# Kernel tuning notes

Measured on AMD Instinct MI355X. Metric: run time of the kernel, lower is better.

## Reference

```python
import jax, jax.numpy as jnp
import numpy as np

DIM = 1024
NUM_HEADS = 16
HEAD_DIM = DIM // NUM_HEADS
BATCH = 64
SEQ = 256


def rope_tables(seq_len, head_dim, dtype=jnp.float32):
    inv_freq = 1.0 / (10000.0 ** (jnp.arange(0, head_dim, 2, dtype=jnp.float32) / head_dim))
    pos = jnp.arange(seq_len, dtype=jnp.float32)
    freqs = jnp.outer(pos, inv_freq)            # (S, head_dim/2)
    emb = jnp.concatenate([freqs, freqs], -1)   # (S, head_dim)
    return jnp.cos(emb).astype(dtype), jnp.sin(emb).astype(dtype)


def rotate_half(x):
    x1, x2 = jnp.split(x, 2, axis=-1)
    return jnp.concatenate([-x2, x1], axis=-1)


def setup_inputs() -> dict:
    key = jax.random.key(0)
    ks = jax.random.split(key, 5)
    x = jax.random.normal(ks[0], (BATCH, SEQ, DIM), dtype=jnp.float32)
    mask = jnp.ones((BATCH, SEQ), dtype=jnp.int32)
    s = 1.0 / np.sqrt(DIM)
    Wq = jax.random.normal(ks[1], (DIM, DIM), dtype=jnp.float32) * s
    Wk = jax.random.normal(ks[2], (DIM, DIM), dtype=jnp.float32) * s
    Wv = jax.random.normal(ks[3], (DIM, DIM), dtype=jnp.float32) * s
    Wo = jax.random.normal(ks[4], (DIM, DIM), dtype=jnp.float32) * s
    return {"x": x, "mask": mask, "Wq": Wq, "Wk": Wk, "Wv": Wv, "Wo": Wo}


def reference(x, mask, Wq, Wk, Wv, Wo):
    B, S, D = x.shape
    H, Hd = NUM_HEADS, HEAD_DIM
    scale = Hd ** -0.5
    # torch nn.Linear: y = x @ W^T  (weights stored as (out,in))
    q = (x @ Wq.T).reshape(B, S, H, Hd).transpose(0, 2, 1, 3)  # (B,H,S,Hd)
    k = (x @ Wk.T).reshape(B, S, H, Hd).transpose(0, 2, 1, 3)
    v = (x @ Wv.T).reshape(B, S, H, Hd).transpose(0, 2, 1, 3)
    cos, sin = rope_tables(S, Hd, x.dtype)       # (S,Hd)
    cos = cos[None, None]                         # (1,1,S,Hd)
    sin = sin[None, None]
    q = q * cos + rotate_half(q) * sin
    k = k * cos + rotate_half(k) * sin
    scores = jnp.einsum('bhqd,bhkd->bhqk', q, k) * scale  # (B,H,S,S)
    m = (mask[:, None, None, :] != 0)             # (B,1,1,S)
    scores = jnp.where(m, scores, -jnp.inf)
    attn = jax.nn.softmax(scores, axis=-1)
    out = jnp.einsum('bhqk,bhkd->bhqd', attn, v)  # (B,H,S,Hd)
    out = out.transpose(0, 2, 1, 3).reshape(B, S, D)
    return out @ Wo.T
```

## Files before the change

### kernel.cpp

```cpp
#include <hip/hip_runtime.h>

typedef __attribute__((ext_vector_type(8))) short short8;
typedef __attribute__((ext_vector_type(4))) float f32x4;

#define DEV __device__ __forceinline__

DEV unsigned short f2bf(float f) {
    unsigned int u = __float_as_uint(f);
    u += 0x7FFFu + ((u >> 16) & 1u);
    return (unsigned short)(u >> 16);
}
DEV float bf2f(unsigned short h) { return __uint_as_float(((unsigned int)h) << 16); }

DEV void gload16(const void* g, void* l) {
    __builtin_amdgcn_global_load_lds(
        (const __attribute__((address_space(1))) void*)(unsigned long long)g,
        (__attribute__((address_space(3))) void*)(unsigned int)(unsigned long long)l,
        16, 0, 0);
}

DEV void cast8(const float* in, unsigned short* out, size_t idx8) {
    const f32x4* p = (const f32x4*)in + idx8 * 2;
    f32x4 a = p[0], b = p[1];
    short8 v;
    v[0] = (short)f2bf(a[0]); v[1] = (short)f2bf(a[1]); v[2] = (short)f2bf(a[2]); v[3] = (short)f2bf(a[3]);
    v[4] = (short)f2bf(b[0]); v[5] = (short)f2bf(b[1]); v[6] = (short)f2bf(b[2]); v[7] = (short)f2bf(b[3]);
    *(short8*)(out + idx8 * 8) = v;
}

__global__ void init_kernel(const float* __restrict__ x,
                            const float* __restrict__ w0, const float* __restrict__ w1,
                            const float* __restrict__ w2, const float* __restrict__ w3,
                            unsigned short* __restrict__ xb,
                            unsigned short* __restrict__ o0, unsigned short* __restrict__ o1,
                            unsigned short* __restrict__ o2, unsigned short* __restrict__ o3,
                            float* __restrict__ cosT, float* __restrict__ sinT) {
    int blk = blockIdx.x;
    int tid = threadIdx.x;
    if (blk < 8192) {
        cast8(x, xb, (size_t)blk * 256 + tid);
    } else if (blk < 8192 + 2048) {
        int gid = (blk - 8192) * 256 + tid;
        int sel = gid >> 17, idx = gid & 131071;
        const float* in = (sel == 0) ? w0 : (sel == 1) ? w1 : (sel == 2) ? w2 : w3;
        unsigned short* out = (sel == 0) ? o0 : (sel == 1) ? o1 : (sel == 2) ? o2 : o3;
        cast8(in, out, (size_t)idx);
    } else {
        int gid = (blk - 8192 - 2048) * 256 + tid;
        if (gid < 256 * 32) {
            int s = gid >> 5, i = gid & 31;
            float inv = powf(10000.0f, -(float)i * (1.0f / 32.0f));
            float f = (float)s * inv;
            cosT[gid] = cosf(f);
            sinT[gid] = sinf(f);
        }
    }
}

#define NT0 16

#define Ald(B, K) (SLDS + ((B) * 2 + (K)) * 8192)
#define Bld(B, K) (SLDS + 32768 + ((B) * 2 + (K)) * 8192)

#define STAGE2(SW, SBUF, SKH, TS) do {                                         \
    int ts_ = (TS) < NT0 ? (TS) : (NT0 - 1);                                   \
    const unsigned short* sp_ = SW##base + (size_t)ts_ * 64 + (SKH) * 32;      \
    gload16(sp_ + rel0, SW##ld(SBUF, SKH) + (size_t)tid * 8);                  \
    gload16(sp_ + rel1, SW##ld(SBUF, SKH) + (size_t)(tid + 512) * 8);          \
} while (0)

#define MM(MH, MI, NI)                                                         \
    acc[(MH)*4+(MI)][(NI)] = __builtin_amdgcn_mfma_f32_16x16x32_bf16(          \
        av##MI, bva[(NI)], acc[(MH)*4+(MI)][(NI)], 0, 0, 0)

#define PH0(BUF, KH, MH, SW, SBUF, SKH, TS, DW) do {                           \
    short8 av0 = *(const short8*)&Ald(BUF, KH)[aoff[(MH)*4 + 0]];              \
    short8 av1 = *(const short8*)&Ald(BUF, KH)[aoff[(MH)*4 + 1]];              \
    short8 av2 = *(const short8*)&Ald(BUF, KH)[aoff[(MH)*4 + 2]];              \
    short8 av3 = *(const short8*)&Ald(BUF, KH)[aoff[(MH)*4 + 3]];              \
    if ((MH) == 0) {                                                           \
        bva[0] = *(const short8*)&Bld(BUF, KH)[boff[0]];                       \
        bva[1] = *(const short8*)&Bld(BUF, KH)[boff[1]];                       \
        bva[2] = *(const short8*)&Bld(BUF, KH)[boff[2]];                       \
        bva[3] = *(const short8*)&Bld(BUF, KH)[boff[3]];                       \
    }                                                                          \
    STAGE2(SW, SBUF, SKH, TS);                                                 \
    if (DW) asm volatile("s_waitcnt vmcnt(8)" ::: "memory");                   \
    asm volatile("" ::: "memory");                                             \
    __builtin_amdgcn_s_barrier();                                              \
    asm volatile("" ::: "memory");                                             \
    __builtin_amdgcn_s_setprio(1);                                             \
    MM(MH,0,0); MM(MH,1,0); MM(MH,2,0); MM(MH,3,0);                            \
    MM(MH,0,1); MM(MH,1,1); MM(MH,2,1); MM(MH,3,1);                            \
    MM(MH,0,2); MM(MH,1,2); MM(MH,2,2); MM(MH,3,2);                            \
    MM(MH,0,3); MM(MH,1,3); MM(MH,2,3); MM(MH,3,3);                            \
    __builtin_amdgcn_s_setprio(0);                                             \
    asm volatile("" ::: "memory");                                             \
    __builtin_amdgcn_s_barrier();                                              \
    asm volatile("" ::: "memory");                                             \
} while (0)

#define TILE0(BUF, T)                                                          \
    PH0(BUF, 0, 0, A, (BUF)^1, 1, (T)+1, 0);                                   \
    PH0(BUF, 0, 1, B, (BUF)^1, 1, (T)+1, 1);                                   \
    PH0(BUF, 1, 0, A, (BUF),   0, (T)+2, 0);                                   \
    PH0(BUF, 1, 1, B, (BUF),   0, (T)+2, 1);

template <int MODE>
__global__ __launch_bounds__(512, 2) void gemm256_kernel(
    const unsigned short* __restrict__ A,
    const unsigned short* __restrict__ W0,
    const unsigned short* __restrict__ W1,
    const unsigned short* __restrict__ W2,
    unsigned short* __restrict__ q,
    unsigned short* __restrict__ k,
    unsigned short* __restrict__ vt,
    float* __restrict__ outF,
    const float* __restrict__ cosT,
    const float* __restrict__ sinT)
{
    __shared__ __align__(16) unsigned short SLDS[65536];

    const int tid = threadIdx.x;
    const int l = tid & 63;
    const int w = tid >> 6;
    const int wr = w >> 2, wc = w & 3;
    const int l15 = l & 15, lg = l >> 4;

    const int nwg = gridDim.x;
    const int bid = blockIdx.x;
    const int cpx = nwg >> 3;
    const int swz = (bid & 7) * cpx + (bid >> 3);
    const int NBX = (MODE == 0) ? 12 : 4;
    const int bx = swz % NBX, by = swz / NBX;
    const int m0 = by * 256, n0 = bx * 256;

    const unsigned short* Bp;
    int nb = n0, sel = 3;
    if (MODE == 0) {
        sel = n0 >> 10;
        Bp = (sel == 0) ? W0 : ((sel == 1) ? W1 : W2);
        nb = n0 & 1023;
    } else {
        Bp = W0;
    }

    const int f0 = tid, f1 = tid + 512;
    const int rel0 = (f0 >> 2) * 1024 + (((f0 & 3) ^ ((f0 >> 3) & 3)) * 8);
    const int rel1 = (f1 >> 2) * 1024 + (((f1 & 3) ^ ((f1 >> 3) & 3)) * 8);
    const unsigned short* Abase = A + (size_t)m0 * 1024;
    const unsigned short* Bbase = Bp + (size_t)nb * 1024;

    int aoff[8], boff[4];
#pragma unroll
    for (int mi = 0; mi < 8; ++mi) {
        int row = wr * 128 + mi * 16 + l15;
        aoff[mi] = row * 32 + ((lg ^ ((row >> 1) & 3)) * 8);
    }
#pragma unroll
    for (int ni = 0; ni < 4; ++ni) {
        int row = wc * 64 + ni * 16 + l15;
        boff[ni] = row * 32 + ((lg ^ ((row >> 1) & 3)) * 8);
    }

    f32x4 acc[8][4];
#pragma unroll
    for (int mi = 0; mi < 8; ++mi)
#pragma unroll
        for (int ni = 0; ni < 4; ++ni)
#pragma unroll
            for (int e = 0; e < 4; ++e) acc[mi][ni][e] = 0.f;

    short8 bva[4];

    STAGE2(A, 0, 0, 0); STAGE2(B, 0, 0, 0);
    STAGE2(A, 0, 1, 0); STAGE2(B, 0, 1, 0);
    STAGE2(A, 1, 0, 1); STAGE2(B, 1, 0, 1);
    asm volatile("s_waitcnt vmcnt(8)" ::: "memory");
    asm volatile("" ::: "memory");
    __builtin_amdgcn_s_barrier();
    asm volatile("" ::: "memory");

#pragma unroll 1
    for (int it = 0; it < NT0 / 2; ++it) {
        const int t0 = it * 2;
        TILE0(0, t0);
        TILE0(1, t0 + 1);
    }

    if (MODE == 1) {
#pragma unroll
        for (int mi = 0; mi < 8; ++mi) {
#pragma unroll
            for (int i = 0; i < 4; ++i) {
                int grow = m0 + wr * 128 + mi * 16 + lg * 4 + i;
#pragma unroll
                for (int ni = 0; ni < 4; ++ni) {
                    int col = n0 + wc * 64 + ni * 16 + l15;
                    outF[(size_t)grow * 1024 + col] = acc[mi][ni][i];
                }
            }
        }
        return;
    }

    asm volatile("s_waitcnt vmcnt(0)" ::: "memory");
    __syncthreads();

    const int b = m0 >> 8;

    if (sel < 2) {
#pragma unroll
        for (int mi = 0; mi < 8; ++mi) {
#pragma unroll
            for (int i = 0; i < 4; ++i) {
                int srow = wr * 128 + mi * 16 + lg * 4 + i;
                int s = srow & 255;
#pragma unroll
                for (int ni = 0; ni < 2; ++ni) {
                    int d = ni * 16 + l15;
                    float c = cosT[s * 32 + d], sn = sinT[s * 32 + d];
                    float lo = acc[mi][ni][i], hi = acc[mi][ni + 2][i];
                    acc[mi][ni][i] = lo * c - hi * sn;
                    acc[mi][ni + 2][i] = hi * c + lo * sn;
                }
#pragma unroll
                for (int ni = 0; ni < 4; ++ni) {
                    int col = wc * 64 + ni * 16 + l15;
                    int byte = srow * 512 + ((col * 2) ^ ((srow & 7) << 4));
                    *(unsigned short*)((char*)SLDS + byte) = f2bf(acc[mi][ni][i]);
                }
            }
        }
    } else {
#pragma unroll
        for (int mi = 0; mi < 8; ++mi) {
#pragma unroll
            for (int i = 0; i < 4; ++i) {
                int srow = wr * 128 + mi * 16 + lg * 4 + i;
#pragma unroll
                for (int ni = 0; ni < 4; ++ni) {
                    int col = wc * 64 + ni * 16 + l15;
                    int byte = col * 512 + ((srow * 2) ^ ((col & 7) << 4));
                    *(unsigned short*)((char*)SLDS + byte) = f2bf(acc[mi][ni][i]);
                }
            }
        }
    }
    __syncthreads();

    {
        const int r = tid >> 5, ct = tid & 31;
        unsigned short* dst01 = (sel == 0) ? q : k;
#pragma unroll
        for (int rg = 0; rg < 16; ++rg) {
            int row = rg * 16 + r;
            int byte = row * 512 + ((ct * 16) ^ ((row & 7) << 4));
            short8 v = *(const short8*)((char*)SLDS + byte);
            if (sel < 2) {
                int col = ct * 8;
                int h = (nb + col) >> 6, d = col & 63;
                *(short8*)(dst01 + (((size_t)(b * 16 + h) * 256 + row) * 64 + d)) = v;
            } else {
                int gc = nb + row;
                int h = gc >> 6, d = gc & 63;
                *(short8*)(vt + (((size_t)(b * 16 + h) * 64 + d) * 256 + ct * 8)) = v;
            }
        }
    }
}

__global__ __launch_bounds__(512) void attn_kernel(
    const unsigned short* __restrict__ qp,
    const unsigned short* __restrict__ kp,
    const unsigned short* __restrict__ vtp,
    const int* __restrict__ mask,
    unsigned short* __restrict__ ao)
{
    __shared__ __align__(16) unsigned short Ks[128 * 64];
    __shared__ __align__(16) unsigned short Vts[64 * 128];
    __shared__ __align__(16) unsigned short Ps[8][32 * 64];

    const int bh = blockIdx.x;
    const int b = bh >> 4, h = bh & 15;
    const int tid = threadIdx.x;
    const int l = tid & 63, w = tid >> 6;
    const int l15 = l & 15, lg = l >> 4;

    const unsigned short* kbase = kp + (size_t)bh * (256 * 64);
    const unsigned short* vtbase = vtp + (size_t)bh * (64 * 256);
    const unsigned short* qbase = qp + (size_t)bh * (256 * 64) + (size_t)(w * 32) * 64;

    short8 aq[2][2];
#pragma unroll
    for (int m = 0; m < 2; ++m)
#pragma unroll
        for (int ks = 0; ks < 2; ++ks)
            aq[m][ks] = *(const short8*)(qbase + (m * 16 + l15) * 64 + ks * 32 + lg * 8);

    float m_run[2][4], l_run[2][4];
    f32x4 o[2][4];
#pragma unroll
    for (int m = 0; m < 2; ++m)
#pragma unroll
        for (int i = 0; i < 4; ++i) { m_run[m][i] = -3.0e38f; l_run[m][i] = 0.f; }
#pragma unroll
    for (int m = 0; m < 2; ++m)
#pragma unroll
        for (int n = 0; n < 4; ++n)
#pragma unroll
            for (int e = 0; e < 4; ++e) o[m][n][e] = 0.f;

    const int* mrow = mask + b * 256;

    for (int half = 0; half < 2; ++half) {
        __syncthreads();
        for (int c2 = tid; c2 < 1024; c2 += 512) {
            int off = c2 * 16;
            int row = off >> 7, cb = off & 127;
            short8 v = *(const short8*)((const char*)kbase + (size_t)half * 16384 + off);
            *(short8*)((char*)Ks + row * 128 + (cb ^ ((row & 7) << 4))) = v;
        }
        for (int c2 = tid; c2 < 1024; c2 += 512) {
            int off = c2 * 16;
            int row = off >> 8, cb = off & 255;
            short8 v = *(const short8*)((const char*)vtbase + (size_t)row * 512 + half * 256 + cb);
            *(short8*)((char*)Vts + row * 256 + (cb ^ ((row & 7) << 4))) = v;
        }
        __syncthreads();

        for (int t2 = 0; t2 < 2; ++t2) {
            const int keyl = t2 * 64;
            const int keyg = half * 128 + keyl;

            f32x4 sf[2][4];
#pragma unroll
            for (int m = 0; m < 2; ++m)
#pragma unroll
                for (int n = 0; n < 4; ++n)
#pragma unroll
                    for (int e = 0; e < 4; ++e) sf[m][n][e] = 0.f;
#pragma unroll
            for (int ks = 0; ks < 2; ++ks) {
                short8 bk[4];
#pragma unroll
                for (int n = 0; n < 4; ++n) {
                    int row = keyl + n * 16 + l15;
                    int cb = (ks * 64 + lg * 16) ^ ((row & 7) << 4);
                    bk[n] = *(const short8*)((char*)Ks + row * 128 + cb);
                }
#pragma unroll
                for (int m = 0; m < 2; ++m)
#pragma unroll
                    for (int n = 0; n < 4; ++n)
                        sf[m][n] = __builtin_amdgcn_mfma_f32_16x16x32_bf16(aq[m][ks], bk[n], sf[m][n], 0, 0, 0);
            }
            float madd[4];
#pragma unroll
            for (int n = 0; n < 4; ++n) madd[n] = mrow[keyg + n * 16 + l15] ? 0.f : -1e30f;
#pragma unroll
            for (int m = 0; m < 2; ++m)
#pragma unroll
                for (int n = 0; n < 4; ++n)
#pragma unroll
                    for (int i = 0; i < 4; ++i) sf[m][n][i] = sf[m][n][i] * 0.125f + madd[n];
            float al[2][4];
#pragma unroll
            for (int m = 0; m < 2; ++m)
#pragma unroll
                for (int i = 0; i < 4; ++i) {
                    float mx = fmaxf(fmaxf(sf[m][0][i], sf[m][1][i]), fmaxf(sf[m][2][i], sf[m][3][i]));
                    mx = fmaxf(mx, __shfl_xor(mx, 1));
                    mx = fmaxf(mx, __shfl_xor(mx, 2));
                    mx = fmaxf(mx, __shfl_xor(mx, 4));
                    mx = fmaxf(mx, __shfl_xor(mx, 8));
                    float mnew = fmaxf(m_run[m][i], mx);
                    al[m][i] = __expf(m_run[m][i] - mnew);
                    m_run[m][i] = mnew;
                }
            float rs[2][4];
#pragma unroll
            for (int m = 0; m < 2; ++m)
#pragma unroll
                for (int i = 0; i < 4; ++i) rs[m][i] = 0.f;
#pragma unroll
            for (int m = 0; m < 2; ++m)
#pragma unroll
                for (int n = 0; n < 4; ++n)
#pragma unroll
                    for (int i = 0; i < 4; ++i) {
                        float p = __expf(sf[m][n][i] - m_run[m][i]);
                        sf[m][n][i] = p;
                        rs[m][i] += p;
                    }
#pragma unroll
            for (int m = 0; m < 2; ++m)
#pragma unroll
                for (int i = 0; i < 4; ++i) {
                    float r2 = rs[m][i];
                    r2 += __shfl_xor(r2, 1);
                    r2 += __shfl_xor(r2, 2);
                    r2 += __shfl_xor(r2, 4);
                    r2 += __shfl_xor(r2, 8);
                    l_run[m][i] = l_run[m][i] * al[m][i] + r2;
                }
#pragma unroll
            for (int m = 0; m < 2; ++m)
#pragma unroll
                for (int n = 0; n < 4; ++n)
#pragma unroll
                    for (int i = 0; i < 4; ++i) o[m][n][i] *= al[m][i];

#pragma unroll
            for (int m = 0; m < 2; ++m)
#pragma unroll
                for (int n = 0; n < 4; ++n)
#pragma unroll
                    for (int i = 0; i < 4; ++i) {
                        int row = m * 16 + lg * 4 + i;
                        int cb = ((n * 16 + l15) * 2) ^ ((row & 7) << 4);
                        *(unsigned short*)((char*)Ps[w] + row * 128 + cb) = f2bf(sf[m][n][i]);
                    }
#pragma unroll
            for (int ks = 0; ks < 2; ++ks) {
                short8 pa[2];
#pragma unroll
                for (int m = 0; m < 2; ++m) {
                    int row = m * 16 + l15;
                    int cb = (ks * 64 + lg * 16) ^ ((row & 7) << 4);
                    pa[m] = *(const short8*)((char*)Ps[w] + row * 128 + cb);
                }
                short8 vb[4];
#pragma unroll
                for (int n = 0; n < 4; ++n) {
                    int row = n * 16 + l15;
                    int cb = (keyl * 2 + ks * 64 + lg * 16) ^ ((row & 7) << 4);
                    vb[n] = *(const short8*)((char*)Vts + row * 256 + cb);
                }
#pragma unroll
                for (int m = 0; m < 2; ++m)
#pragma unroll
                    for (int n = 0; n < 4; ++n)
                        o[m][n] = __builtin_amdgcn_mfma_f32_16x16x32_bf16(pa[m], vb[n], o[m][n], 0, 0, 0);
            }
        }
    }

    unsigned short* aop = ao + ((size_t)(b * 256 + w * 32)) * 1024 + h * 64;
#pragma unroll
    for (int m = 0; m < 2; ++m)
#pragma unroll
        for (int n = 0; n < 4; ++n)
#pragma unroll
            for (int i = 0; i < 4; ++i) {
                int row = m * 16 + lg * 4 + i;
                int d = n * 16 + l15;
                aop[(size_t)row * 1024 + d] = f2bf(o[m][n][i] / l_run[m][i]);
            }
}

extern "C" void kernel_launch(void* const* d_in, const int* in_sizes, int n_in,
                              void* d_out, int out_size, void* d_ws, size_t ws_size,
                              hipStream_t stream) {
    const float* x = (const float*)d_in[0];
    const int* mask = (const int*)d_in[1];
    const float* Wq = (const float*)d_in[2];
    const float* Wk = (const float*)d_in[3];
    const float* Wv = (const float*)d_in[4];
    const float* Wo = (const float*)d_in[5];
    float* out = (float*)d_out;

    char* ws = (char*)d_ws;
    size_t off = 0;
    auto alloc = [&](size_t bytes) -> char* {
        char* p = ws + off;
        off = (off + bytes + 255) & ~(size_t)255;
        return p;
    };
    unsigned short* xb = (unsigned short*)alloc((size_t)16384 * 1024 * 2);
    unsigned short* wqb = (unsigned short*)alloc((size_t)1024 * 1024 * 2);
    unsigned short* wkb = (unsigned short*)alloc((size_t)1024 * 1024 * 2);
    unsigned short* wvb = (unsigned short*)alloc((size_t)1024 * 1024 * 2);
    unsigned short* wob = (unsigned short*)alloc((size_t)1024 * 1024 * 2);
    unsigned short* q = (unsigned short*)alloc((size_t)16384 * 1024 * 2);
    unsigned short* k = (unsigned short*)alloc((size_t)16384 * 1024 * 2);
    unsigned short* vt = (unsigned short*)alloc((size_t)16384 * 1024 * 2);
    float* cosT = (float*)alloc(256 * 32 * 4);
    float* sinT = (float*)alloc(256 * 32 * 4);

    init_kernel<<<8192 + 2048 + 32, 256, 0, stream>>>(x, Wq, Wk, Wv, Wo,
                                                      xb, wqb, wkb, wvb, wob, cosT, sinT);

    gemm256_kernel<0><<<768, 512, 0, stream>>>(xb, wqb, wkb, wvb, q, k, vt, nullptr, cosT, sinT);
    attn_kernel<<<1024, 512, 0, stream>>>(q, k, vt, mask, xb );
    gemm256_kernel<1><<<256, 512, 0, stream>>>(xb, wob, nullptr, nullptr, nullptr, nullptr, nullptr, out, cosT, sinT);

    (void)in_sizes; (void)n_in; (void)out_size; (void)ws_size;
}
```

Baseline: 243.2 us.

## Read K and V^T fragments directly from global memory instead of LDS staging

The attention kernel no longer stages K and V^T tiles into shared memory with block-wide barriers. Each wave now loads its MFMA B-operand fragments straight from global memory, relying on L1/L2 caching since all 8 waves read the same K/V data. This removes the __syncthreads and the LDS round trip and frees LDS for higher occupancy, but it replaces shared reuse with eight-fold redundant global/cache traffic and exposes global load latency right before the MFMAs.

```diff
diff --git a/kernel.cpp b/kernel.cpp
--- a/kernel.cpp
+++ b/kernel.cpp
@@ -277,8 +277,6 @@
     const int* __restrict__ mask,
     unsigned short* __restrict__ ao)
 {
-    __shared__ __align__(16) unsigned short Ks[128 * 64];
-    __shared__ __align__(16) unsigned short Vts[64 * 128];
     __shared__ __align__(16) unsigned short Ps[8][32 * 64];
 
     const int bh = blockIdx.x;
@@ -313,136 +311,113 @@
 
     const int* mrow = mask + b * 256;
 
-    for (int half = 0; half < 2; ++half) {
-        __syncthreads();
-        for (int c2 = tid; c2 < 1024; c2 += 512) {
-            int off = c2 * 16;
-            int row = off >> 7, cb = off & 127;
-            short8 v = *(const short8*)((const char*)kbase + (size_t)half * 16384 + off);
-            *(short8*)((char*)Ks + row * 128 + (cb ^ ((row & 7) << 4))) = v;
-        }
-        for (int c2 = tid; c2 < 1024; c2 += 512) {
-            int off = c2 * 16;
-            int row = off >> 8, cb = off & 255;
-            short8 v = *(const short8*)((const char*)vtbase + (size_t)row * 512 + half * 256 + cb);
-            *(short8*)((char*)Vts + row * 256 + (cb ^ ((row & 7) << 4))) = v;
-        }
-        __syncthreads();
-
-        for (int t2 = 0; t2 < 2; ++t2) {
-            const int keyl = t2 * 64;
-            const int keyg = half * 128 + keyl;
-
-            f32x4 sf[2][4];
+#pragma unroll 1
+    for (int t2 = 0; t2 < 4; ++t2) {
+        const int keyg = t2 * 64;
+
+        f32x4 sf[2][4];
+#pragma unroll
+        for (int m = 0; m < 2; ++m)
+#pragma unroll
+            for (int n = 0; n < 4; ++n)
+#pragma unroll
+                for (int e = 0; e < 4; ++e) sf[m][n][e] = 0.f;
+#pragma unroll
+        for (int ks = 0; ks < 2; ++ks) {
+            short8 bk[4];
+#pragma unroll
+            for (int n = 0; n < 4; ++n)
+                bk[n] = *(const short8*)(kbase + (size_t)(keyg + n * 16 + l15) * 64 + ks * 32 + lg * 8);
 #pragma unroll
             for (int m = 0; m < 2; ++m)
 #pragma unroll
                 for (int n = 0; n < 4; ++n)
-#pragma unroll
-                    for (int e = 0; e < 4; ++e) sf[m][n][e] = 0.f;
-#pragma unroll
-            for (int ks = 0; ks < 2; ++ks) {
-                short8 bk[4];
-#pragma unroll
-                for (int n = 0; n < 4; ++n) {
-                    int row = keyl + n * 16 + l15;
-                    int cb = (ks * 64 + lg * 16) ^ ((row & 7) << 4);
-                    bk[n] = *(const short8*)((char*)Ks + row * 128 + cb);
-                }
-#pragma unroll
-                for (int m = 0; m < 2; ++m)
-#pragma unroll
-                    for (int n = 0; n < 4; ++n)
-                        sf[m][n] = __builtin_amdgcn_mfma_f32_16x16x32_bf16(aq[m][ks], bk[n], sf[m][n], 0, 0, 0);
-            }
-            float madd[4];
-#pragma unroll
-            for (int n = 0; n < 4; ++n) madd[n] = mrow[keyg + n * 16 + l15] ? 0.f : -1e30f;
+                    sf[m][n] = __builtin_amdgcn_mfma_f32_16x16x32_bf16(aq[m][ks], bk[n], sf[m][n], 0, 0, 0);
+        }
+        float madd[4];
+#pragma unroll
+        for (int n = 0; n < 4; ++n) madd[n] = mrow[keyg + n * 16 + l15] ? 0.f : -1e30f;
+#pragma unroll
+        for (int m = 0; m < 2; ++m)
+#pragma unroll
+            for (int n = 0; n < 4; ++n)
+#pragma unroll
+                for (int i = 0; i < 4; ++i) sf[m][n][i] = sf[m][n][i] * 0.125f + madd[n];
+        float al[2][4];
+#pragma unroll
+        for (int m = 0; m < 2; ++m)
+#pragma unroll
+            for (int i = 0; i < 4; ++i) {
+                float mx = fmaxf(fmaxf(sf[m][0][i], sf[m][1][i]), fmaxf(sf[m][2][i], sf[m][3][i]));
+                mx = fmaxf(mx, __shfl_xor(mx, 1));
+                mx = fmaxf(mx, __shfl_xor(mx, 2));
+                mx = fmaxf(mx, __shfl_xor(mx, 4));
+                mx = fmaxf(mx, __shfl_xor(mx, 8));
+                float mnew = fmaxf(m_run[m][i], mx);
+                al[m][i] = __expf(m_run[m][i] - mnew);
+                m_run[m][i] = mnew;
+            }
+        float rs[2][4];
+#pragma unroll
+        for (int m = 0; m < 2; ++m)
+#pragma unroll
+            for (int i = 0; i < 4; ++i) rs[m][i] = 0.f;
+#pragma unroll
+        for (int m = 0; m < 2; ++m)
+#pragma unroll
+            for (int n = 0; n < 4; ++n)
+#pragma unroll
+                for (int i = 0; i < 4; ++i) {
+                    float p = __expf(sf[m][n][i] - m_run[m][i]);
+                    sf[m][n][i] = p;
+                    rs[m][i] += p;
+                }
+#pragma unroll
+        for (int m = 0; m < 2; ++m)
+#pragma unroll
+            for (int i = 0; i < 4; ++i) {
+                float r2 = rs[m][i];
+                r2 += __shfl_xor(r2, 1);
+                r2 += __shfl_xor(r2, 2);
+                r2 += __shfl_xor(r2, 4);
+                r2 += __shfl_xor(r2, 8);
+                l_run[m][i] = l_run[m][i] * al[m][i] + r2;
+            }
+#pragma unroll
+        for (int m = 0; m < 2; ++m)
+#pragma unroll
+            for (int n = 0; n < 4; ++n)
+#pragma unroll
+                for (int i = 0; i < 4; ++i) o[m][n][i] *= al[m][i];
+
+#pragma unroll
+        for (int m = 0; m < 2; ++m)
+#pragma unroll
+            for (int n = 0; n < 4; ++n)
+#pragma unroll
+                for (int i = 0; i < 4; ++i) {
+                    int row = m * 16 + lg * 4 + i;
+                    int cb = ((n * 16 + l15) * 2) ^ ((row & 7) << 4);
+                    *(unsigned short*)((char*)Ps[w] + row * 128 + cb) = f2bf(sf[m][n][i]);
+                }
+#pragma unroll
+        for (int ks = 0; ks < 2; ++ks) {
+            short8 pa[2];
+#pragma unroll
+            for (int m = 0; m < 2; ++m) {
+                int row = m * 16 + l15;
+                int cb = (ks * 64 + lg * 16) ^ ((row & 7) << 4);
+                pa[m] = *(const short8*)((char*)Ps[w] + row * 128 + cb);
+            }
+            short8 vb[4];
+#pragma unroll
+            for (int n = 0; n < 4; ++n)
+                vb[n] = *(const short8*)(vtbase + (size_t)(n * 16 + l15) * 256 + keyg + ks * 32 + lg * 8);
 #pragma unroll
             for (int m = 0; m < 2; ++m)
 #pragma unroll
                 for (int n = 0; n < 4; ++n)
-#pragma unroll
-                    for (int i = 0; i < 4; ++i) sf[m][n][i] = sf[m][n][i] * 0.125f + madd[n];
-            float al[2][4];
-#pragma unroll
-            for (int m = 0; m < 2; ++m)
-#pragma unroll
-                for (int i = 0; i < 4; ++i) {
-                    float mx = fmaxf(fmaxf(sf[m][0][i], sf[m][1][i]), fmaxf(sf[m][2][i], sf[m][3][i]));
-                    mx = fmaxf(mx, __shfl_xor(mx, 1));
-                    mx = fmaxf(mx, __shfl_xor(mx, 2));
-                    mx = fmaxf(mx, __shfl_xor(mx, 4));
-                    mx = fmaxf(mx, __shfl_xor(mx, 8));
-                    float mnew = fmaxf(m_run[m][i], mx);
-                    al[m][i] = __expf(m_run[m][i] - mnew);
-                    m_run[m][i] = mnew;
-                }
-            float rs[2][4];
-#pragma unroll
-            for (int m = 0; m < 2; ++m)
-#pragma unroll
-                for (int i = 0; i < 4; ++i) rs[m][i] = 0.f;
-#pragma unroll
-            for (int m = 0; m < 2; ++m)
-#pragma unroll
-                for (int n = 0; n < 4; ++n)
-#pragma unroll
-                    for (int i = 0; i < 4; ++i) {
-                        float p = __expf(sf[m][n][i] - m_run[m][i]);
-                        sf[m][n][i] = p;
-                        rs[m][i] += p;
-                    }
-#pragma unroll
-            for (int m = 0; m < 2; ++m)
-#pragma unroll
-                for (int i = 0; i < 4; ++i) {
-                    float r2 = rs[m][i];
-                    r2 += __shfl_xor(r2, 1);
-                    r2 += __shfl_xor(r2, 2);
-                    r2 += __shfl_xor(r2, 4);
-                    r2 += __shfl_xor(r2, 8);
-                    l_run[m][i] = l_run[m][i] * al[m][i] + r2;
-                }
-#pragma unroll
-            for (int m = 0; m < 2; ++m)
-#pragma unroll
-                for (int n = 0; n < 4; ++n)
-#pragma unroll
-                    for (int i = 0; i < 4; ++i) o[m][n][i] *= al[m][i];
-
-#pragma unroll
-            for (int m = 0; m < 2; ++m)
-#pragma unroll
-                for (int n = 0; n < 4; ++n)
-#pragma unroll
-                    for (int i = 0; i < 4; ++i) {
-                        int row = m * 16 + lg * 4 + i;
-                        int cb = ((n * 16 + l15) * 2) ^ ((row & 7) << 4);
-                        *(unsigned short*)((char*)Ps[w] + row * 128 + cb) = f2bf(sf[m][n][i]);
-                    }
-#pragma unroll
-            for (int ks = 0; ks < 2; ++ks) {
-                short8 pa[2];
-#pragma unroll
-                for (int m = 0; m < 2; ++m) {
-                    int row = m * 16 + l15;
-                    int cb = (ks * 64 + lg * 16) ^ ((row & 7) << 4);
-                    pa[m] = *(const short8*)((char*)Ps[w] + row * 128 + cb);
-                }
-                short8 vb[4];
-#pragma unroll
-                for (int n = 0; n < 4; ++n) {
-                    int row = n * 16 + l15;
-                    int cb = (keyl * 2 + ks * 64 + lg * 16) ^ ((row & 7) << 4);
-                    vb[n] = *(const short8*)((char*)Vts + row * 256 + cb);
-                }
-#pragma unroll
-                for (int m = 0; m < 2; ++m)
-#pragma unroll
-                    for (int n = 0; n < 4; ++n)
-                        o[m][n] = __builtin_amdgcn_mfma_f32_16x16x32_bf16(pa[m], vb[n], o[m][n], 0, 0, 0);
-            }
+                    o[m][n] = __builtin_amdgcn_mfma_f32_16x16x32_bf16(pa[m], vb[n], o[m][n], 0, 0, 0);
         }
     }
 
```

After: 247.8 us. About the same (+1.9%).
